# Kernel tuning notes

Measured on AMD Instinct MI355X. Metric: run time of the kernel, lower is better.

The kernel has to match this reference:

```python
import jax, jax.numpy as jnp
import numpy as np

IL = 9          # input_length
TL = 29         # total_length
P = TL - IL     # pred_length = 20
H = 512
W = 512


def _gather(imgs, yi, xi):
    # imgs: [B,1,H,W], yi/xi: [B,H,W] int32 -> [B,1,H,W]
    return jax.vmap(lambda im, y, x: im[0][y, x])(imgs, yi, xi)[:, None]


def _bilinear(imgs, cy, cx):
    # border padding, align_corners=True: coords already clipped to [0,dim-1]
    x0 = jnp.floor(cx)
    y0 = jnp.floor(cy)
    wx = (cx - x0)[:, None]  # [B,1,H,W]
    wy = (cy - y0)[:, None]
    x0i = jnp.clip(x0.astype(jnp.int32), 0, W - 1)
    y0i = jnp.clip(y0.astype(jnp.int32), 0, H - 1)
    x1i = jnp.clip(x0i + 1, 0, W - 1)
    y1i = jnp.clip(y0i + 1, 0, H - 1)
    v00 = _gather(imgs, y0i, x0i)
    v01 = _gather(imgs, y0i, x1i)
    v10 = _gather(imgs, y1i, x0i)
    v11 = _gather(imgs, y1i, x1i)
    return (1 - wy) * ((1 - wx) * v00 + wx * v01) + wy * ((1 - wx) * v10 + wx * v11)


def _nearest(imgs, cy, cx):
    # torch grid_sample 'nearest' uses round-half-to-even, same as jnp.round
    yi = jnp.clip(jnp.round(cy).astype(jnp.int32), 0, H - 1)
    xi = jnp.clip(jnp.round(cx).astype(jnp.int32), 0, W - 1)
    return _gather(imgs, yi, xi)


def setup_inputs() -> dict:
    key = jax.random.key(0)
    k1, k2, k3 = jax.random.split(key, 3)
    all_frames = jax.random.uniform(k1, (8, TL, H, W, 1), dtype=jnp.float32)
    motion = jax.random.normal(k2, (8, P * 2, H, W), dtype=jnp.float32)
    intensity = jax.random.normal(k3, (8, P, H, W), dtype=jnp.float32)
    return {"all_frames": all_frames, "motion": motion, "intensity": intensity}


def reference(all_frames, motion, intensity):
    all_frames = all_frames[:, :, :, :, :1]
    B = all_frames.shape[0]
    # last observed frame: [B,1,H,W]
    last = all_frames[:, IL - 1:IL, :, :, 0]
    motion_ = motion.reshape(B, P, 2, H, W)
    intensity_ = intensity.reshape(B, P, 1, H, W)

    gy, gx = jnp.meshgrid(jnp.arange(H, dtype=jnp.float32),
                          jnp.arange(W, dtype=jnp.float32), indexing="ij")

    def step(carry, xs):
        flow, inten = xs  # [B,2,H,W], [B,1,H,W]
        cx = jnp.clip(gx + flow[:, 0], 0.0, W - 1)
        cy = jnp.clip(gy + flow[:, 1], 0.0, H - 1)
        bili = _bilinear(carry, cy, cx)
        nxt = _nearest(carry, cy, cx) + inten
        return nxt, (nxt, bili)

    xs = (jnp.swapaxes(motion_, 0, 1), jnp.swapaxes(intensity_, 0, 1))
    _, (series, bilis) = jax.lax.scan(step, last, xs)
    # series/bilis: [P,B,1,H,W] -> [B,P,H,W]
    evo_result = jnp.swapaxes(series, 0, 1).reshape(B, P, H, W) / 128.0
    evo_motion = jnp.swapaxes(bilis, 0, 1).reshape(B, P, H, W)
    return evo_result, evo_motion, motion_
```

## Files before the change

### kernel.cpp

```cpp
#include <hip/hip_runtime.h>

#define W_  512
#define H_  512
#define HW  (512 * 512)
#define P_  20
#define B_  8
#define TL_ 29
#define IL_ 9

#define NT  256
#define NBLK 4096
#define HALF (HW / 2)

__global__ __launch_bounds__(NT) void step_kernel(
    const float* __restrict__ prev_base,
    long prev_stride,
    float prev_scale,
    const float* __restrict__ motion,
    const float* __restrict__ intensity,
    float* __restrict__ evo_result,
    float* __restrict__ evo_motion,
    float* __restrict__ motion_out,
    int p)
{
    const int b    = blockIdx.x & 7;
    const int base = ((blockIdx.x >> 3) << 8) + threadIdx.x;

    const float* prev = prev_base + (long)b * prev_stride;
    const long moP = ((long)b * (2 * P_) + 2 * p) * HW;
    const long ioP = ((long)b * P_ + p) * HW;

    #pragma unroll
    for (int j = 0; j < 2; ++j) {
        const int rem = base + j * HALF;
        const int y   = rem >> 9;
        const int x   = rem & (W_ - 1);

        const long mo0 = moP + rem;
        const long io  = ioP + rem;

        const float f0 = __builtin_nontemporal_load(motion + mo0);
        const float f1 = __builtin_nontemporal_load(motion + mo0 + HW);
        const float iv = __builtin_nontemporal_load(intensity + io);

        __builtin_nontemporal_store(f0, motion_out + mo0);
        __builtin_nontemporal_store(f1, motion_out + mo0 + HW);

        const float cx = fminf(fmaxf((float)x + f0, 0.0f), 511.0f);
        const float cy = fminf(fmaxf((float)y + f1, 0.0f), 511.0f);

        const float x0f = floorf(cx), y0f = floorf(cy);
        const float wx = cx - x0f, wy = cy - y0f;
        const int x0 = (int)x0f, y0 = (int)y0f;
        const int x1 = min(x0 + 1, W_ - 1), y1 = min(y0 + 1, H_ - 1);

        const float* r0 = prev + y0 * W_;
        const float* r1 = prev + y1 * W_;
        const float v00 = r0[x0], v01 = r0[x1];
        const float v10 = r1[x0], v11 = r1[x1];
        const float bil = prev_scale * ((1.0f - wy) * ((1.0f - wx) * v00 + wx * v01)
                                              + wy  * ((1.0f - wx) * v10 + wx * v11));

        const int xi = (int)rintf(cx);
        const int yi = (int)rintf(cy);
        const float res = (prev_scale * prev[yi * W_ + xi] + iv) * 0.0078125f;

        evo_result[io] = res;
        __builtin_nontemporal_store(bil, evo_motion + io);
    }
}

extern "C" void kernel_launch(void* const* d_in, const int* in_sizes, int n_in,
                              void* d_out, int out_size, void* d_ws, size_t ws_size,
                              hipStream_t stream)
{
    const float* frames    = (const float*)d_in[0];
    const float* motion    = (const float*)d_in[1];
    const float* intensity = (const float*)d_in[2];

    float* out        = (float*)d_out;
    float* evo_result = out;
    float* evo_motion = out + (long)B_ * P_ * HW;
    float* motion_out = out + 2L * B_ * P_ * HW;

    step_kernel<<<NBLK, NT, 0, stream>>>(
        frames + (long)(IL_ - 1) * HW, (long)TL_ * HW, 1.0f,
        motion, intensity, evo_result, evo_motion, motion_out, 0);

    for (int p = 1; p < P_; ++p) {
        step_kernel<<<NBLK, NT, 0, stream>>>(
            evo_result + (long)(p - 1) * HW, (long)P_ * HW, 128.0f,
            motion, intensity, evo_result, evo_motion, motion_out, p);
    }
}
```

Before: 335.0 us.

## Fuse 20 step launches into one persistent kernel with per-batch grid barriers

```diff
diff --git a/kernel.cpp b/kernel.cpp
--- a/kernel.cpp
+++ b/kernel.cpp
@@ -8,65 +8,143 @@
 #define TL_ 29
 #define IL_ 9
 
-#define NT  256
-#define NBLK 4096
-#define HALF (HW / 2)
+#define NB   1024
+#define NT   256
+#define BPB  (NB / B_)
+#define TPB  (BPB * NT)
+#define PPT  (HW / TPB)
 
-__global__ __launch_bounds__(NT) void step_kernel(
-    const float* __restrict__ prev_base,
-    long prev_stride,
-    float prev_scale,
+#define WS_MISMATCH 0
+#define WS_GCNT     32
+#define WS_GGO      64
+#define WS_SCNT     96
+#define WS_SGO      128
+#define WS_FBAR(b)  (160 + 32 * (b))
+#define WS_FGO(b)   (448 + 32 * (b))
+
+__device__ __forceinline__ unsigned rel_faa(unsigned* p, unsigned v) {
+    return __hip_atomic_fetch_add(p, v, __ATOMIC_RELAXED, __HIP_MEMORY_SCOPE_AGENT);
+}
+__device__ __forceinline__ void rel_st(unsigned* p, unsigned v) {
+    __hip_atomic_store(p, v, __ATOMIC_RELAXED, __HIP_MEMORY_SCOPE_AGENT);
+}
+__device__ __forceinline__ unsigned rel_ld(unsigned* p) {
+    return __hip_atomic_load(p, __ATOMIC_RELAXED, __HIP_MEMORY_SCOPE_AGENT);
+}
+__device__ __forceinline__ float mall_ldf(const float* p) {
+    return __hip_atomic_load(p, __ATOMIC_RELAXED, __HIP_MEMORY_SCOPE_AGENT);
+}
+__device__ __forceinline__ void mall_stf(float* p, float v) {
+    __hip_atomic_store(p, v, __ATOMIC_RELAXED, __HIP_MEMORY_SCOPE_AGENT);
+}
+
+__global__ __launch_bounds__(NT, 4) void fused_scan(
+    const float* __restrict__ frames,
     const float* __restrict__ motion,
     const float* __restrict__ intensity,
-    float* __restrict__ evo_result,
-    float* __restrict__ evo_motion,
-    float* __restrict__ motion_out,
-    int p)
+    float*                    evo_result,
+    float* __restrict__       evo_motion,
+    float* __restrict__       motion_out,
+    unsigned*                 ws)
 {
-    const int b    = blockIdx.x & 7;
-    const int base = ((blockIdx.x >> 3) << 8) + threadIdx.x;
+    const int bid = blockIdx.x;
+    const int b   = bid & 7;
+    const int inb = ((bid >> 3) << 8) + threadIdx.x;
 
-    const float* prev = prev_base + (long)b * prev_stride;
-    const long moP = ((long)b * (2 * P_) + 2 * p) * HW;
-    const long ioP = ((long)b * P_ + p) * HW;
+    __shared__ unsigned s_flag;
+    if (threadIdx.x == 0) {
+        unsigned xcc;
+        asm volatile("s_getreg_b32 %0, hwreg(HW_REG_XCC_ID)" : "=s"(xcc));
+        if ((int)(xcc & 7) != b) rel_st(ws + WS_MISMATCH, 1u);
+        asm volatile("s_waitcnt vmcnt(0)" ::: "memory");
+    }
+    __syncthreads();
+    if (threadIdx.x == 0) {
+        unsigned old = rel_faa(ws + WS_GCNT, 1u);
+        if (old + 1 == NB) rel_st(ws + WS_GGO, 1u);
+        else while (rel_ld(ws + WS_GGO) < 1u) __builtin_amdgcn_s_sleep(2);
+        s_flag = rel_ld(ws + WS_MISMATCH);
+        asm volatile("" ::: "memory");
+    }
+    __syncthreads();
+    const bool fast = (s_flag == 0);
 
-    #pragma unroll
-    for (int j = 0; j < 2; ++j) {
-        const int rem = base + j * HALF;
-        const int y   = rem >> 9;
-        const int x   = rem & (W_ - 1);
+    const float* frame0 = frames + ((long)b * TL_ + (IL_ - 1)) * HW;
 
-        const long mo0 = moP + rem;
-        const long io  = ioP + rem;
+    for (int p = 0; p < P_; ++p) {
+        const float scale = (p == 0) ? 1.0f : 128.0f;
+        const float* prev = (p == 0) ? frame0
+                                     : evo_result + ((long)b * P_ + (p - 1)) * HW;
+        const long moP = ((long)b * (2 * P_) + 2 * p) * HW;
+        const long ioP = ((long)b * P_ + p) * HW;
 
-        const float f0 = __builtin_nontemporal_load(motion + mo0);
-        const float f1 = __builtin_nontemporal_load(motion + mo0 + HW);
-        const float iv = __builtin_nontemporal_load(intensity + io);
+        for (int j = 0; j < PPT; ++j) {
+            const int rem = j * TPB + inb;
+            const int y   = rem >> 9;
+            const int x   = rem & (W_ - 1);
+            const long mo0 = moP + rem;
+            const long io  = ioP + rem;
 
-        __builtin_nontemporal_store(f0, motion_out + mo0);
-        __builtin_nontemporal_store(f1, motion_out + mo0 + HW);
+            const float f0 = __builtin_nontemporal_load(motion + mo0);
+            const float f1 = __builtin_nontemporal_load(motion + mo0 + HW);
+            const float iv = __builtin_nontemporal_load(intensity + io);
+            __builtin_nontemporal_store(f0, motion_out + mo0);
+            __builtin_nontemporal_store(f1, motion_out + mo0 + HW);
 
-        const float cx = fminf(fmaxf((float)x + f0, 0.0f), 511.0f);
-        const float cy = fminf(fmaxf((float)y + f1, 0.0f), 511.0f);
+            const float cx = fminf(fmaxf((float)x + f0, 0.0f), 511.0f);
+            const float cy = fminf(fmaxf((float)y + f1, 0.0f), 511.0f);
+            const float x0f = floorf(cx), y0f = floorf(cy);
+            const float wx = cx - x0f, wy = cy - y0f;
+            const int x0 = (int)x0f, y0 = (int)y0f;
+            const int x1 = min(x0 + 1, W_ - 1), y1 = min(y0 + 1, H_ - 1);
+            const int xi = (int)rintf(cx);
+            const int yi = (int)rintf(cy);
 
-        const float x0f = floorf(cx), y0f = floorf(cy);
-        const float wx = cx - x0f, wy = cy - y0f;
-        const int x0 = (int)x0f, y0 = (int)y0f;
-        const int x1 = min(x0 + 1, W_ - 1), y1 = min(y0 + 1, H_ - 1);
+            float v00, v01, v10, v11, vn;
+            if (p == 0) {
+                v00 = prev[y0 * W_ + x0];  v01 = prev[y0 * W_ + x1];
+                v10 = prev[y1 * W_ + x0];  v11 = prev[y1 * W_ + x1];
+                vn  = prev[yi * W_ + xi];
+            } else if (fast) {
+                v00 = prev[y0 * W_ + x0];  v01 = prev[y0 * W_ + x1];
+                v10 = prev[y1 * W_ + x0];  v11 = prev[y1 * W_ + x1];
+                vn  = prev[yi * W_ + xi];
+            } else {
+                v00 = mall_ldf(prev + y0 * W_ + x0);
+                v01 = mall_ldf(prev + y0 * W_ + x1);
+                v10 = mall_ldf(prev + y1 * W_ + x0);
+                v11 = mall_ldf(prev + y1 * W_ + x1);
+                vn  = mall_ldf(prev + yi * W_ + xi);
+            }
 
-        const float* r0 = prev + y0 * W_;
-        const float* r1 = prev + y1 * W_;
-        const float v00 = r0[x0], v01 = r0[x1];
-        const float v10 = r1[x0], v11 = r1[x1];
-        const float bil = prev_scale * ((1.0f - wy) * ((1.0f - wx) * v00 + wx * v01)
-                                              + wy  * ((1.0f - wx) * v10 + wx * v11));
+            const float bil = scale * ((1.0f - wy) * ((1.0f - wx) * v00 + wx * v01)
+                                             + wy  * ((1.0f - wx) * v10 + wx * v11));
+            const float res = (scale * vn + iv) * 0.0078125f;
 
-        const int xi = (int)rintf(cx);
-        const int yi = (int)rintf(cy);
-        const float res = (prev_scale * prev[yi * W_ + xi] + iv) * 0.0078125f;
+            if (fast) evo_result[io] = res;
+            else      mall_stf(evo_result + io, res);
+            __builtin_nontemporal_store(bil, evo_motion + io);
+        }
 
-        evo_result[io] = res;
-        __builtin_nontemporal_store(bil, evo_motion + io);
+        if (p != P_ - 1) {
+            __syncthreads();
+            if (threadIdx.x == 0) {
+                const unsigned gen = (unsigned)(p + 1);
+                if (fast) {
+                    unsigned old = rel_faa(ws + WS_FBAR(b), 1u);
+                    if (old + 1 == gen * BPB) rel_st(ws + WS_FGO(b), gen);
+                    else while (rel_ld(ws + WS_FGO(b)) < gen)
+                        __builtin_amdgcn_s_sleep(2);
+                } else {
+                    unsigned old = rel_faa(ws + WS_SCNT, 1u);
+                    if (old + 1 == gen * NB) rel_st(ws + WS_SGO, gen);
+                    else while (rel_ld(ws + WS_SGO) < gen)
+                        __builtin_amdgcn_s_sleep(2);
+                }
+                asm volatile("" ::: "memory");
+            }
+            __syncthreads();
+        }
     }
 }
 
@@ -82,14 +160,10 @@
     float* evo_result = out;
     float* evo_motion = out + (long)B_ * P_ * HW;
     float* motion_out = out + 2L * B_ * P_ * HW;
+    unsigned* ws      = (unsigned*)d_ws;
 
-    step_kernel<<<NBLK, NT, 0, stream>>>(
-        frames + (long)(IL_ - 1) * HW, (long)TL_ * HW, 1.0f,
-        motion, intensity, evo_result, evo_motion, motion_out, 0);
+    hipMemsetAsync(ws, 0, 4096, stream);
 
-    for (int p = 1; p < P_; ++p) {
-        step_kernel<<<NBLK, NT, 0, stream>>>(
-            evo_result + (long)(p - 1) * HW, (long)P_ * HW, 128.0f,
-            motion, intensity, evo_result, evo_motion, motion_out, p);
-    }
+    fused_scan<<<dim3(NB), dim3(NT), 0, stream>>>(
+        frames, motion, intensity, evo_result, evo_motion, motion_out, ws);
 }
```

New measurement: 376.4 us. 12.4% more time.
